# Kernel optimization log

Measured on AMD Instinct MI355X. Metric: run time of the kernel, lower is better.

The kernel has to match this reference:

```python
import jax, jax.numpy as jnp
import numpy as np

B = 32; N = 512; SEQ_LEN = 8
L = 0.05; T_REF = 5.0; V_TH = 20.0; V_RES = 0.0
SQL = float(np.sqrt(L))
BN_EPS = 1e-5

# ---- Dawson-style lookup tables for the LIF moment activation (built once, float64) ----
_XG = np.linspace(-10.0, 4.0, 7001)
_DX = _XG[1] - _XG[0]

def _cumtrapz(y):
    return np.concatenate([[0.0], np.cumsum(0.5 * (y[1:] + y[:-1]) * _DX)])

_phi = np.exp(-_XG ** 2)
_I = np.exp(-100.0) / 20.0 + _cumtrapz(_phi)          # int_{-inf}^x e^{-t^2} dt (asymptotic tail at -10)
_g = np.exp(_XG ** 2) * _I                             # 1st Dawson-like function g(x)
_G = _cumtrapz(_g)                                     # int g dx (rel. to -10)
_h = np.exp(_XG ** 2) * _cumtrapz(_phi * _g ** 2)      # 2nd Dawson-like function h(x)
_H = _cumtrapz(_h)                                     # int h dx

XG = jnp.asarray(_XG, jnp.float32)
GT = jnp.asarray(_g, jnp.float32)
GI = jnp.asarray(_G, jnp.float32)
HI = jnp.asarray(_H, jnp.float32)

def _interp(x, tab):
    return jnp.interp(x, XG, tab)

def moment_activate(u, s, rho):
    # Mnn_Activate_Mean / Std / Corr: LIF moment activation
    s = jnp.maximum(s, 1e-6)
    ub = jnp.clip((V_TH * L - u) / (s * SQL), -10.0, 4.0)
    lb = jnp.clip((V_RES * L - u) / (s * SQL), -10.0, 4.0)
    dG = _interp(ub, GI) - _interp(lb, GI)
    ua = 1.0 / (T_REF + (2.0 / L) * dG)                               # mean firing rate
    dH = jnp.maximum(_interp(ub, HI) - _interp(lb, HI), 0.0)
    sa = jnp.sqrt((8.0 / L ** 2) * dH * ua ** 3)                      # firing std
    dg = _interp(ub, GT) - _interp(lb, GT)
    chi = ua ** 2 * (2.0 / L) * dg / (SQL * jnp.maximum(sa, 1e-9))    # linear response coeff
    eye = jnp.eye(rho.shape[-1], dtype=rho.dtype)
    rho_out = chi[:, :, None] * chi[:, None, :] * rho                 # [B,N,N]
    rho_out = rho_out * (1.0 - eye) + eye                             # unit diagonal
    return ua, sa, rho_out

def linear_corr(W, b, u, s, rho):
    # Mnn_Linear_Corr: mean via affine map, covariance via W C W^T
    u_out = u @ W.T + b
    Cin = rho * s[:, :, None] * s[:, None, :]                         # [B,N,N] covariance
    C = jnp.einsum('bik,lk->bil', jnp.einsum('ij,bjk->bik', W, Cin), W)
    var = jnp.clip(jnp.diagonal(C, axis1=1, axis2=2), 0.0, None)
    s_out = jnp.sqrt(var)
    denom = s_out[:, :, None] * s_out[:, None, :]
    rho_out = jnp.where(denom > 1e-12, C / jnp.maximum(denom, 1e-12), 0.0)
    return u_out, s_out, rho_out

def mexi_hat(n, k=0.3):
    dx = 2.0 * np.pi / n
    x = np.arange(0.0, 2.0 * np.pi, dx)[:n]
    y = np.exp(2.0 * (np.cos(x) - 1.0)) * np.cos(2.0 * x)
    j = np.arange(n)
    idx = (j[None, :] - j[:, None]) % n                               # w[i,:] = y.roll(i)
    return y[idx].astype(np.float32)

def setup_inputs() -> dict:
    ks = jax.random.split(jax.random.key(0), 10)
    u = jax.random.normal(ks[0], (B, N), jnp.float32)
    s = jax.random.uniform(ks[1], (B, N), jnp.float32, 0.1, 1.0)
    A = jax.random.normal(ks[2], (B, N, N), jnp.float32) / np.sqrt(N)
    sym = 0.5 * (A + jnp.swapaxes(A, 1, 2))
    eye = jnp.eye(N, dtype=jnp.float32)
    rho = jnp.clip(sym, -0.5, 0.5) * (1.0 - eye) + eye                # valid-ish corr matrix
    u_ext = jax.random.normal(ks[3], (B, N), jnp.float32)
    s_ext = jax.random.uniform(ks[4], (B, N), jnp.float32, 0.1, 1.0)
    W = 0.02 * jax.random.normal(ks[5], (N, N), jnp.float32) + 0.1 * jnp.asarray(mexi_hat(N))
    b = 0.02 * jax.random.normal(ks[6], (N,), jnp.float32)
    W_ext = 0.02 * jax.random.normal(ks[7], (N, N), jnp.float32)
    b_ext = 0.02 * jax.random.normal(ks[8], (N,), jnp.float32)
    w_mean = 2.5 * jnp.ones((N,), jnp.float32)
    b_mean = 2.5 * jnp.ones((N,), jnp.float32)
    w_mean_ext = 2.5 * jnp.ones((N,), jnp.float32)
    b_mean_ext = 2.5 * jnp.ones((N,), jnp.float32)
    return {'u': u, 's': s, 'rho': rho, 'u_ext': u_ext, 's_ext': s_ext,
            'W': W, 'b': b, 'W_ext': W_ext, 'b_ext': b_ext,
            'w_mean': w_mean, 'b_mean': b_mean,
            'w_mean_ext': w_mean_ext, 'b_mean_ext': b_mean_ext,
            'seq_len': SEQ_LEN}

def reference(u, s, rho, u_ext, s_ext, W, b, W_ext, b_ext,
              w_mean, b_mean, w_mean_ext, b_mean_ext, seq_len):
    # external pathway (Mnn_Linear_without_Corr + BN), computed once
    u_e = u_ext @ W_ext.T + b_ext
    s_e = jnp.sqrt((s_ext ** 2) @ (W_ext ** 2).T)
    mean_e = jnp.mean(u_e, axis=0); var_e = jnp.var(u_e, axis=0)
    f_e = w_mean_ext / jnp.sqrt(var_e + BN_EPS)
    s_e = s_e * jnp.abs(f_e)                                          # Mnn_Std_Bn1d (uses pre-BN stats)
    u_e = (u_e - mean_e) * f_e + b_mean_ext

    def step(carry, _):
        u, s, rho = carry
        u, s, rho = linear_corr(W, b, u, s, rho)
        mean = jnp.mean(u, axis=0); var = jnp.var(u, axis=0)
        f = w_mean / jnp.sqrt(var + BN_EPS)
        s = s * jnp.abs(f)
        u = (u - mean) * f + b_mean
        u = u + u_e
        s = jnp.sqrt(s * s + s_e * s_e)
        return moment_activate(u, s, rho), None

    (u, s, rho), _ = jax.lax.scan(step, (u, s, rho), None, length=seq_len)
    return u, s, rho
```

## Files before the change

kernel.cpp:

```cpp
#include <hip/hip_runtime.h>
#include <math.h>


#define BB 32
#define NN 512
#define SEQ 8
#define TG 7001

typedef float f32x4 __attribute__((ext_vector_type(4)));
typedef short s16x8 __attribute__((ext_vector_type(8)));

__device__ __forceinline__ unsigned short bf16_rne(float v) {
    unsigned u = __float_as_uint(v);
    u += 0x7FFFu + ((u >> 16) & 1u);
    return (unsigned short)(u >> 16);
}
__device__ __forceinline__ float bf16_f(unsigned short h) {
    return __uint_as_float(((unsigned)h) << 16);
}
__device__ __forceinline__ void split2(float v, unsigned short& h, unsigned short& l) {
    unsigned short hh = bf16_rne(v);
    h = hh;
    l = bf16_rne(v - bf16_f(hh));
}

__device__ __forceinline__ size_t ts_idx(int r, int k) {
    return (size_t)(((r >> 4) * 16 + (k >> 5)) * 512 + ((k >> 3) & 3) * 128 + (r & 15) * 8 + (k & 7));
}

__device__ __forceinline__ float interp_tab(const float* __restrict__ tab, float x) {
    float t = (x + 10.0f) * 500.0f;
    t = fminf(fmaxf(t, 0.0f), 7000.0f);
    int i0 = (int)t;
    if (i0 > 6999) i0 = 6999;
    float fr = t - (float)i0;
    float a = tab[i0];
    float b = tab[i0 + 1];
    return a + fr * (b - a);
}

__global__ void k_exp(double* __restrict__ expP, double* __restrict__ expM) {
    int k = blockIdx.x * 256 + threadIdx.x;
    if (k >= TG) return;
    double x = -10.0 + (14.0 / 7000.0) * k;
    expP[k] = exp(x * x);
    expM[k] = exp(-x * x);
}

__device__ double blk_exscan(double part, double* wsum) {
    int t = threadIdx.x, lane = t & 63, wid = t >> 6;
    double run = part;
    #pragma unroll
    for (int off = 1; off < 64; off <<= 1) {
        double nv = __shfl_up(run, off);
        if (lane >= off) run += nv;
    }
    if (lane == 63) wsum[wid] = run;
    __syncthreads();
    if (t < 16) {
        double v = wsum[t];
        #pragma unroll
        for (int off = 1; off < 16; off <<= 1) {
            double nv = __shfl_up(v, off);
            if (lane >= off) v += nv;
        }
        wsum[t] = v;
    }
    __syncthreads();
    double base = (wid > 0) ? wsum[wid - 1] : 0.0;
    double ex = base + run - part;
    __syncthreads();
    return ex;
}

__global__ __launch_bounds__(1024)
void k_scan(const double* __restrict__ expP, const double* __restrict__ expM,
            float* __restrict__ GT, float* __restrict__ GI, float* __restrict__ HI) {
    __shared__ double ys[7008];
    __shared__ double wsum[16];
    const int t = threadIdx.x;
    const double dx = 14.0 / 7000.0;
    int k0 = t * 7, k1 = k0 + 7;
    if (k1 > TG) k1 = TG;
    if (k0 > TG) k0 = TG;
    int kls = (k0 < 1) ? 1 : k0;

    for (int k = k0; k < k1; ++k) ys[k] = expM[k];
    __syncthreads();

    double tmp[7];
    {
        double part = 0.0;
        for (int k = kls; k < k1; ++k) part += 0.5 * (ys[k - 1] + ys[k]) * dx;
        double run = blk_exscan(part, wsum) + exp(-100.0) / 20.0;
        int c = 0;
        for (int k = k0; k < k1; ++k) {
            if (k >= 1) run += 0.5 * (ys[k - 1] + ys[k]) * dx;
            tmp[c] = expP[k] * run;
            GT[k] = (float)tmp[c];
            ++c;
        }
        __syncthreads();
        c = 0;
        for (int k = k0; k < k1; ++k) ys[k] = tmp[c++];
        __syncthreads();
    }
    {
        double part = 0.0;
        for (int k = kls; k < k1; ++k) part += 0.5 * (ys[k - 1] + ys[k]) * dx;
        double run = blk_exscan(part, wsum);
        for (int k = k0; k < k1; ++k) {
            if (k >= 1) run += 0.5 * (ys[k - 1] + ys[k]) * dx;
            GI[k] = (float)run;
        }
        __syncthreads();
    }
    {
        double part = 0.0;
        for (int k = kls; k < k1; ++k) {
            double ya = expM[k - 1] * ys[k - 1] * ys[k - 1];
            double yb = expM[k] * ys[k] * ys[k];
            part += 0.5 * (ya + yb) * dx;
        }
        double run = blk_exscan(part, wsum);
        int c = 0;
        for (int k = k0; k < k1; ++k) {
            if (k >= 1) {
                double ya = expM[k - 1] * ys[k - 1] * ys[k - 1];
                double yb = expM[k] * ys[k] * ys[k];
                run += 0.5 * (ya + yb) * dx;
            }
            tmp[c++] = run;
        }
        __syncthreads();
        c = 0;
        for (int k = k0; k < k1; ++k) ys[k] = tmp[c++];
        __syncthreads();
    }
    {
        double part = 0.0;
        for (int k = kls; k < k1; ++k)
            part += 0.5 * (expP[k - 1] * ys[k - 1] + expP[k] * ys[k]) * dx;
        double run = blk_exscan(part, wsum);
        for (int k = k0; k < k1; ++k) {
            if (k >= 1) run += 0.5 * (expP[k - 1] * ys[k - 1] + expP[k] * ys[k]) * dx;
            HI[k] = (float)run;
        }
    }
}

__global__ void k_splitW(const float* __restrict__ W,
                         unsigned short* __restrict__ Wh, unsigned short* __restrict__ Wl) {
    int t = blockIdx.x * 256 + threadIdx.x;
    int r = t >> 6, c8 = t & 63;
    int k = c8 * 8;
    const float* src = W + (size_t)r * NN + k;
    s16x8 hv, lv;
    #pragma unroll
    for (int q = 0; q < 8; ++q) {
        unsigned short h, l;
        split2(src[q], h, l);
        hv[q] = (short)h; lv[q] = (short)l;
    }
    size_t o = ts_idx(r, k);
    *reinterpret_cast<s16x8*>(Wh + o) = hv;
    *reinterpret_cast<s16x8*>(Wl + o) = lv;
}

__global__ void k_splitQ(const float* __restrict__ rho, const float* __restrict__ s,
                         unsigned short* __restrict__ Qh, unsigned short* __restrict__ Ql) {
    int t = blockIdx.x * 256 + threadIdx.x;
    int b = t >> 15;
    int rem = t & 32767;
    int r = rem >> 6, c8 = rem & 63;
    int k = c8 * 8;
    const float* src = rho + ((size_t)b * NN + r) * NN + k;
    const float* sb = s + b * NN;
    float si = sb[r];
    s16x8 hv, lv;
    #pragma unroll
    for (int q = 0; q < 8; ++q) {
        float v = src[q] * si * sb[k + q];
        unsigned short h, l;
        split2(v, h, l);
        hv[q] = (short)h; lv[q] = (short)l;
    }
    size_t o = (size_t)b * NN * NN + ts_idx(r, k);
    *reinterpret_cast<s16x8*>(Qh + o) = hv;
    *reinterpret_cast<s16x8*>(Ql + o) = lv;
}

template <int PHASE>
__global__ __launch_bounds__(256, 2)
void gemm_ts(const unsigned short* __restrict__ Ah, const unsigned short* __restrict__ Al,
             long aStride,
             const unsigned short* __restrict__ Bh, const unsigned short* __restrict__ Bl,
             long bStride,
             unsigned short* __restrict__ Oh, unsigned short* __restrict__ Ol,
             float* __restrict__ Of,
             const float* __restrict__ Wf, float* __restrict__ sv_a, float* __restrict__ sv_b,
             const float* __restrict__ u_prev, const float* __restrict__ bvec,
             float* __restrict__ u_linT,
             const float* __restrict__ bn_w, const float* __restrict__ bmv,
             const float* __restrict__ u_e, const float* __restrict__ s_e2,
             const float* __restrict__ GT, const float* __restrict__ GI,
             const float* __restrict__ HI,
             float* __restrict__ u_next, float* __restrict__ s_next) {
    __shared__ __align__(16) unsigned short stg[4 * 8192];
    __shared__ float slS[256], chS[256], snS[256];

    const int id = blockIdx.x;
    const int member = (id >> 3) & 3;
    const int g = (id & 7) | ((id >> 5) << 3);
    const int p = g & 3;
    const int b = g >> 2;
    const int xt = (PHASE == 0) ? p : member;
    const int yt = (PHASE == 0) ? member : p;
    const int i0 = yt * 128, j0 = xt * 128;
    const int tid = threadIdx.x;
    const int w = tid >> 6, lane = tid & 63;
    const int wqm = w >> 1, wqn = w & 1;

    if (PHASE == 0) {
        const int tile16 = yt * 4 + xt;
        const int row = tile16 * 32 + (tid >> 3);
        const int seg = tid & 7;
        const float4* wr = (const float4*)(Wf + (size_t)row * NN + seg * 64);
        const float4* ur = (const float4*)(u_prev + b * NN + seg * 64);
        float a0 = 0.f, a1 = 0.f, a2 = 0.f, a3 = 0.f;
        #pragma unroll
        for (int kk = 0; kk < 16; ++kk) {
            float4 wv = wr[kk], uv = ur[kk];
            a0 = fmaf(wv.x, uv.x, a0);
            a1 = fmaf(wv.y, uv.y, a1);
            a2 = fmaf(wv.z, uv.z, a2);
            a3 = fmaf(wv.w, uv.w, a3);
        }
        float au = (a0 + a1) + (a2 + a3);
        au += __shfl_xor(au, 1);
        au += __shfl_xor(au, 2);
        au += __shfl_xor(au, 4);
        if (seg == 0) u_linT[row * BB + b] = au + bvec[row];
    } else {
        const int ii = (tid < 128) ? (i0 + tid) : (j0 + tid - 128);
        float vb[32];
        {
            const float4* ul = (const float4*)(u_linT + (size_t)ii * BB);
            #pragma unroll
            for (int q = 0; q < 8; ++q) {
                float4 t4 = ul[q];
                vb[q * 4 + 0] = t4.x; vb[q * 4 + 1] = t4.y;
                vb[q * 4 + 2] = t4.z; vb[q * 4 + 3] = t4.w;
            }
        }
        float m = 0.0f;
        #pragma unroll
        for (int bb = 0; bb < BB; ++bb) m += vb[bb];
        m *= (1.0f / BB);
        float v = 0.0f;
        #pragma unroll
        for (int bb = 0; bb < BB; ++bb) {
            float d = vb[bb] - m;
            v = fmaf(d, d, v);
        }
        v *= (1.0f / BB);
        float f = bn_w[ii] / sqrtf(v + 1e-5f);
        const int idx = b * NN + ii;
        float s_l = sqrtf(fmaxf(sv_a[idx], 0.0f));
        float un = (vb[b] - m) * f + bmv[ii] + u_e[idx];
        float sn = sqrtf(s_l * s_l * f * f + s_e2[idx]);
        const float SQL = 0.22360679774997896f;
        float ss = fmaxf(sn, 1e-6f);
        float inv = 1.0f / (ss * SQL);
        float ubx = fminf(fmaxf((1.0f - un) * inv, -10.0f), 4.0f);
        float lbx = fminf(fmaxf((0.0f - un) * inv, -10.0f), 4.0f);
        float dG = interp_tab(GI, ubx) - interp_tab(GI, lbx);
        float ua = 1.0f / (5.0f + 40.0f * dG);
        float dH = fmaxf(interp_tab(HI, ubx) - interp_tab(HI, lbx), 0.0f);
        float sa = sqrtf(3200.0f * dH * ua * ua * ua);
        float dg2 = interp_tab(GT, ubx) - interp_tab(GT, lbx);
        float ch = ua * ua * 40.0f * dg2 / (SQL * fmaxf(sa, 1e-9f));
        slS[tid] = s_l;
        chS[tid] = ch;
        snS[tid] = sa;
        if (i0 == j0 && tid < 128) {
            u_next[idx] = ua;
            s_next[idx] = sa;
            sv_b[idx] = 0.0f;
        }
        __syncthreads();
    }

    const int laneo = lane * 8;
    const unsigned short* pAh = Ah + (size_t)b * aStride + (size_t)((i0 >> 4) + wqm * 4) * 8192 + laneo;
    const unsigned short* pAl = Al + (size_t)b * aStride + (size_t)((i0 >> 4) + wqm * 4) * 8192 + laneo;
    const unsigned short* pBh = Bh + (size_t)b * bStride + (size_t)((j0 >> 4) + wqn * 4) * 8192 + laneo;
    const unsigned short* pBl = Bl + (size_t)b * bStride + (size_t)((j0 >> 4) + wqn * 4) * 8192 + laneo;

    f32x4 acc[4][4];
    #pragma unroll
    for (int m2 = 0; m2 < 4; ++m2)
        #pragma unroll
        for (int n2 = 0; n2 < 4; ++n2) acc[m2][n2] = (f32x4){0.f, 0.f, 0.f, 0.f};

    #pragma unroll 2
    for (int kb = 0; kb < 16; ++kb) {
        const int off = kb * 512;
        s16x8 ahf[4], alf[4], bhf[4], blf[4];
        #pragma unroll
        for (int t = 0; t < 4; ++t) {
            ahf[t] = *reinterpret_cast<const s16x8*>(pAh + t * 8192 + off);
            alf[t] = *reinterpret_cast<const s16x8*>(pAl + t * 8192 + off);
            bhf[t] = *reinterpret_cast<const s16x8*>(pBh + t * 8192 + off);
            blf[t] = *reinterpret_cast<const s16x8*>(pBl + t * 8192 + off);
        }
        #pragma unroll
        for (int m2 = 0; m2 < 4; ++m2)
            #pragma unroll
            for (int n2 = 0; n2 < 4; ++n2) {
                acc[m2][n2] = __builtin_amdgcn_mfma_f32_16x16x32_bf16(ahf[m2], bhf[n2], acc[m2][n2], 0, 0, 0);
                acc[m2][n2] = __builtin_amdgcn_mfma_f32_16x16x32_bf16(ahf[m2], blf[n2], acc[m2][n2], 0, 0, 0);
                acc[m2][n2] = __builtin_amdgcn_mfma_f32_16x16x32_bf16(alf[m2], bhf[n2], acc[m2][n2], 0, 0, 0);
            }
    }

    const size_t bofs = (size_t)b * NN * NN;
    const int rb0 = i0 + wqm * 64 + (lane >> 4) * 4;
    const int cb0 = j0 + wqn * 64 + (lane & 15);

    if (PHASE == 0) {
        float dp[16];
        #pragma unroll
        for (int m2 = 0; m2 < 4; ++m2)
            #pragma unroll
            for (int r = 0; r < 4; ++r) {
                int row = rb0 + m2 * 16 + r;
                const float* wrow = Wf + ((size_t)row << 9) + cb0;
                float s = 0.0f;
                #pragma unroll
                for (int n2 = 0; n2 < 4; ++n2) s = fmaf(acc[m2][n2][r], wrow[n2 * 16], s);
                dp[m2 * 4 + r] = s;
            }
        #pragma unroll
        for (int k = 0; k < 16; ++k) {
            #pragma unroll
            for (int off = 1; off < 16; off <<= 1) dp[k] += __shfl_xor(dp[k], off);
        }
        if ((lane & 15) == 0) {
            #pragma unroll
            for (int k = 0; k < 16; ++k) {
                int row = rb0 + (k >> 2) * 16 + (k & 3);
                atomicAdd(&sv_a[b * NN + row], dp[k]);
            }
        }
    }

    if (PHASE == 2) {
        float* fS = (float*)stg + w * 4096;
        const int lcf = ((lane >> 4) << 8) + (lane & 15);
        #pragma unroll
        for (int m2 = 0; m2 < 4; ++m2)
            #pragma unroll
            for (int r = 0; r < 4; ++r) {
                const int lr = m2 * 16 + (lane >> 4) * 4 + r;
                const float si = slS[wqm * 64 + lr], ci = chS[wqm * 64 + lr];
                const int row = i0 + wqm * 64 + lr;
                #pragma unroll
                for (int n2 = 0; n2 < 4; ++n2) {
                    const int lc = wqn * 64 + n2 * 16 + (lane & 15);
                    const float sj = slS[128 + lc], cj = chS[128 + lc];
                    const int col = j0 + lc;
                    float denom = si * sj;
                    float rv = (denom > 1e-12f) ? (acc[m2][n2][r] / fmaxf(denom, 1e-12f)) : 0.0f;
                    rv *= ci * cj;
                    if (row == col) rv = 1.0f;
                    fS[lcf + m2 * 1024 + r * 64 + n2 * 16] = rv;
                }
            }
        #pragma unroll
        for (int inst = 0; inst < 16; ++inst) {
            const int row = i0 + wqm * 64 + inst * 4 + (lane >> 4);
            const int col = j0 + wqn * 64 + (lane & 15) * 4;
            *reinterpret_cast<f32x4*>(Of + bofs + ((size_t)row << 9) + col) =
                *reinterpret_cast<const f32x4*>(fS + inst * 256 + (lane >> 4) * 64 + (lane & 15) * 4);
        }
    } else {
        unsigned short* hiS = stg + w * 8192;
        unsigned short* loS = hiS + 4096;
        const int laneconst = (((lane & 15) >> 3) << 7) + ((lane >> 4) << 5) + (lane & 7);
        #pragma unroll
        for (int m2 = 0; m2 < 4; ++m2)
            #pragma unroll
            for (int n2 = 0; n2 < 4; ++n2) {
                const int base = laneconst + m2 * 1024 + (n2 >> 1) * 512 + (n2 & 1) * 256;
                #pragma unroll
                for (int r = 0; r < 4; ++r) {
                    float v;
                    if (PHASE == 0) {
                        v = acc[m2][n2][r];
                    } else {
                        const int lr = wqm * 64 + m2 * 16 + (lane >> 4) * 4 + r;
                        const int lc = wqn * 64 + n2 * 16 + (lane & 15);
                        const float si = slS[lr], ci = chS[lr], qi = snS[lr];
                        const float sj = slS[128 + lc], cj = chS[128 + lc], qj = snS[128 + lc];
                        float denom = si * sj;
                        float rv = (denom > 1e-12f) ? (acc[m2][n2][r] / fmaxf(denom, 1e-12f)) : 0.0f;
                        rv *= ci * cj;
                        if (i0 + lr == j0 + lc) rv = 1.0f;
                        v = rv * qi * qj;
                    }
                    unsigned short h, l;
                    split2(v, h, l);
                    hiS[base + r * 8] = h;
                    loS[base + r * 8] = l;
                }
            }
        #pragma unroll
        for (int lb = 0; lb < 8; ++lb) {
            const int gb = ((i0 >> 4) + wqm * 4 + (lb >> 1)) * 16 + (j0 >> 5) + wqn * 2 + (lb & 1);
            *reinterpret_cast<s16x8*>(Oh + bofs + (size_t)gb * 512 + laneo) =
                *reinterpret_cast<const s16x8*>(hiS + lb * 512 + laneo);
            *reinterpret_cast<s16x8*>(Ol + bofs + (size_t)gb * 512 + laneo) =
                *reinterpret_cast<const s16x8*>(loS + lb * 512 + laneo);
        }
    }
}

__global__ void k_ext_dots(const float* __restrict__ Wx, const float* __restrict__ bx,
                           const float* __restrict__ ux, const float* __restrict__ sx,
                           float* __restrict__ u_e, float* __restrict__ s_e2) {
    int gw = (blockIdx.x << 2) + (threadIdx.x >> 6);
    int lane = threadIdx.x & 63;
    int b = gw >> 9, i = gw & 511;
    const float* wr = Wx + (size_t)i * NN;
    const float* ub = ux + b * NN;
    const float* sb = sx + b * NN;
    float au = 0.0f, as2 = 0.0f;
    for (int j = lane; j < NN; j += 64) {
        float w = wr[j];
        float s = sb[j];
        au = fmaf(w, ub[j], au);
        as2 = fmaf(w * w, s * s, as2);
    }
    #pragma unroll
    for (int off = 32; off; off >>= 1) {
        au += __shfl_down(au, off);
        as2 += __shfl_down(as2, off);
    }
    if (lane == 0) {
        u_e[b * NN + i] = au + bx[i];
        s_e2[b * NN + i] = as2;
    }
}

__global__ void k_ext_stats(float* __restrict__ u_e, float* __restrict__ s_e2,
                            const float* __restrict__ wmx, const float* __restrict__ bmx) {
    int i = blockIdx.x * blockDim.x + threadIdx.x;
    if (i >= NN) return;
    float m = 0.0f;
    for (int b = 0; b < BB; ++b) m += u_e[b * NN + i];
    m *= (1.0f / BB);
    float v = 0.0f;
    for (int b = 0; b < BB; ++b) {
        float d = u_e[b * NN + i] - m;
        v = fmaf(d, d, v);
    }
    v *= (1.0f / BB);
    float f = wmx[i] / sqrtf(v + 1e-5f);
    float bm = bmx[i];
    for (int b = 0; b < BB; ++b) {
        u_e[b * NN + i] = (u_e[b * NN + i] - m) * f + bm;
        s_e2[b * NN + i] *= f * f;
    }
}

extern "C" void kernel_launch(void* const* d_in, const int* in_sizes, int n_in,
                              void* d_out, int out_size, void* d_ws, size_t ws_size,
                              hipStream_t stream) {
    (void)in_sizes; (void)n_in; (void)out_size; (void)ws_size;
    const float* u_in       = (const float*)d_in[0];
    const float* s_in       = (const float*)d_in[1];
    const float* rho_in     = (const float*)d_in[2];
    const float* u_ext      = (const float*)d_in[3];
    const float* s_ext      = (const float*)d_in[4];
    const float* W          = (const float*)d_in[5];
    const float* bvec       = (const float*)d_in[6];
    const float* W_ext      = (const float*)d_in[7];
    const float* b_ext      = (const float*)d_in[8];
    const float* w_mean     = (const float*)d_in[9];
    const float* b_mean     = (const float*)d_in[10];
    const float* w_mean_ext = (const float*)d_in[11];
    const float* b_mean_ext = (const float*)d_in[12];

    float* out_u   = (float*)d_out;
    float* out_s   = out_u + BB * NN;
    float* out_rho = out_s + BB * NN;
    unsigned short* Qh = (unsigned short*)out_rho;
    unsigned short* Ql = Qh + (size_t)BB * NN * NN;

    char* base = (char*)d_ws;
    size_t off = 0;
    auto alloc = [&](size_t bytes) -> char* {
        char* ptr = base + off;
        off += (bytes + 255) & ~(size_t)255;
        return ptr;
    };
    unsigned short* T1h = (unsigned short*)alloc((size_t)BB * NN * NN * 2);
    unsigned short* T1l = (unsigned short*)alloc((size_t)BB * NN * NN * 2);
    unsigned short* Wh  = (unsigned short*)alloc((size_t)NN * NN * 2);
    unsigned short* Wl  = (unsigned short*)alloc((size_t)NN * NN * 2);
    double* expP = (double*)alloc(TG * 8);
    double* expM = (double*)alloc(TG * 8);
    float* GTt   = (float*)alloc(TG * 4);
    float* GIt   = (float*)alloc(TG * 4);
    float* HIt   = (float*)alloc(TG * 4);
    float* u_e   = (float*)alloc(BB * NN * 4);
    float* s_e2  = (float*)alloc(BB * NN * 4);
    float* uA    = (float*)alloc(BB * NN * 4);
    float* uB2   = (float*)alloc(BB * NN * 4);
    float* sA    = (float*)alloc(BB * NN * 4);
    float* sB2   = (float*)alloc(BB * NN * 4);
    float* u_linT = (float*)alloc(BB * NN * 4);
    float* sv0   = (float*)alloc(BB * NN * 4);
    float* sv1   = (float*)alloc(BB * NN * 4);

    k_exp<<<28, 256, 0, stream>>>(expP, expM);
    k_scan<<<1, 1024, 0, stream>>>(expP, expM, GTt, GIt, HIt);
    k_splitW<<<128, 256, 0, stream>>>(W, Wh, Wl);
    k_splitQ<<<4096, 256, 0, stream>>>(rho_in, s_in, Qh, Ql);
    k_ext_dots<<<BB * NN / 4, 256, 0, stream>>>(W_ext, b_ext, u_ext, s_ext, u_e, s_e2);
    k_ext_stats<<<2, 256, 0, stream>>>(u_e, s_e2, w_mean_ext, b_mean_ext);
    (void)hipMemsetAsync(sv0, 0, BB * NN * 4, stream);

    const float* cu = u_in;

    for (int t = 0; t < SEQ; ++t) {
        float* sva = (t & 1) ? sv1 : sv0;
        float* svb = (t & 1) ? sv0 : sv1;
        gemm_ts<0><<<512, 256, 0, stream>>>(
            Wh, Wl, 0L, Qh, Ql, (long)NN * NN, T1h, T1l, nullptr,
            W, sva, nullptr, cu, bvec, u_linT,
            nullptr, nullptr, nullptr, nullptr, nullptr, nullptr, nullptr,
            nullptr, nullptr);
        float* nu = (t == SEQ - 1) ? out_u : ((t & 1) ? uA : uB2);
        float* ns = (t == SEQ - 1) ? out_s : ((t & 1) ? sA : sB2);
        if (t < SEQ - 1) {
            gemm_ts<1><<<512, 256, 0, stream>>>(
                T1h, T1l, (long)NN * NN, Wh, Wl, 0L, Qh, Ql, nullptr,
                nullptr, sva, svb, nullptr, nullptr, u_linT,
                w_mean, b_mean, u_e, s_e2, GTt, GIt, HIt, nu, ns);
        } else {
            gemm_ts<2><<<512, 256, 0, stream>>>(
                T1h, T1l, (long)NN * NN, Wh, Wl, 0L, nullptr, nullptr, out_rho,
                nullptr, sva, svb, nullptr, nullptr, u_linT,
                w_mean, b_mean, u_e, s_e2, GTt, GIt, HIt, nu, ns);
        }
        cu = nu;
    }
}
```

Measured before the change: 759.4 us.

## Use 512-thread blocks with 8 waves per 128x128 tile and swizzled LDS staging

Doubles the threads per GEMM block from 256 to 512, so each of 8 waves computes a 64x32 sub-tile instead of 4 waves doing 64x64. This halves per-wave accumulators and B fragments, lowering register pressure and raising launch bounds to allow more resident waves. The epilogue staging layout is reworked with an XOR swizzle to reduce LDS bank conflicts, and the PHASE 0 mean dot product is split over 16 lanes. In exchange, A fragments are now loaded redundantly by more waves, and half the threads sit idle during the activation prologue.

Measured after the change: 803.4 us. 1.06x slower.

```diff
diff --git a/kernel.cpp b/kernel.cpp
--- a/kernel.cpp
+++ b/kernel.cpp
@@ -191,7 +191,7 @@
 }
 
 template <int PHASE>
-__global__ __launch_bounds__(256, 2)
+__global__ __launch_bounds__(512, 4)
 void gemm_ts(const unsigned short* __restrict__ Ah, const unsigned short* __restrict__ Al,
              long aStride,
              const unsigned short* __restrict__ Bh, const unsigned short* __restrict__ Bl,
@@ -206,7 +206,7 @@
              const float* __restrict__ GT, const float* __restrict__ GI,
              const float* __restrict__ HI,
              float* __restrict__ u_next, float* __restrict__ s_next) {
-    __shared__ __align__(16) unsigned short stg[4 * 8192];
+    __shared__ __align__(16) unsigned short stg[8 * 4096];
     __shared__ float slS[256], chS[256], snS[256];
 
     const int id = blockIdx.x;
@@ -219,17 +219,17 @@
     const int i0 = yt * 128, j0 = xt * 128;
     const int tid = threadIdx.x;
     const int w = tid >> 6, lane = tid & 63;
-    const int wqm = w >> 1, wqn = w & 1;
+    const int wqm = w >> 2, wqn = w & 3;
 
     if (PHASE == 0) {
         const int tile16 = yt * 4 + xt;
-        const int row = tile16 * 32 + (tid >> 3);
-        const int seg = tid & 7;
-        const float4* wr = (const float4*)(Wf + (size_t)row * NN + seg * 64);
-        const float4* ur = (const float4*)(u_prev + b * NN + seg * 64);
+        const int row = tile16 * 32 + (tid >> 4);
+        const int seg = tid & 15;
+        const float4* wr = (const float4*)(Wf + (size_t)row * NN + seg * 32);
+        const float4* ur = (const float4*)(u_prev + b * NN + seg * 32);
         float a0 = 0.f, a1 = 0.f, a2 = 0.f, a3 = 0.f;
         #pragma unroll
-        for (int kk = 0; kk < 16; ++kk) {
+        for (int kk = 0; kk < 8; ++kk) {
             float4 wv = wr[kk], uv = ur[kk];
             a0 = fmaf(wv.x, uv.x, a0);
             a1 = fmaf(wv.y, uv.y, a1);
@@ -240,53 +240,56 @@
         au += __shfl_xor(au, 1);
         au += __shfl_xor(au, 2);
         au += __shfl_xor(au, 4);
+        au += __shfl_xor(au, 8);
         if (seg == 0) u_linT[row * BB + b] = au + bvec[row];
     } else {
-        const int ii = (tid < 128) ? (i0 + tid) : (j0 + tid - 128);
-        float vb[32];
-        {
-            const float4* ul = (const float4*)(u_linT + (size_t)ii * BB);
-            #pragma unroll
-            for (int q = 0; q < 8; ++q) {
-                float4 t4 = ul[q];
-                vb[q * 4 + 0] = t4.x; vb[q * 4 + 1] = t4.y;
-                vb[q * 4 + 2] = t4.z; vb[q * 4 + 3] = t4.w;
-            }
-        }
-        float m = 0.0f;
-        #pragma unroll
-        for (int bb = 0; bb < BB; ++bb) m += vb[bb];
-        m *= (1.0f / BB);
-        float v = 0.0f;
-        #pragma unroll
-        for (int bb = 0; bb < BB; ++bb) {
-            float d = vb[bb] - m;
-            v = fmaf(d, d, v);
-        }
-        v *= (1.0f / BB);
-        float f = bn_w[ii] / sqrtf(v + 1e-5f);
-        const int idx = b * NN + ii;
-        float s_l = sqrtf(fmaxf(sv_a[idx], 0.0f));
-        float un = (vb[b] - m) * f + bmv[ii] + u_e[idx];
-        float sn = sqrtf(s_l * s_l * f * f + s_e2[idx]);
-        const float SQL = 0.22360679774997896f;
-        float ss = fmaxf(sn, 1e-6f);
-        float inv = 1.0f / (ss * SQL);
-        float ubx = fminf(fmaxf((1.0f - un) * inv, -10.0f), 4.0f);
-        float lbx = fminf(fmaxf((0.0f - un) * inv, -10.0f), 4.0f);
-        float dG = interp_tab(GI, ubx) - interp_tab(GI, lbx);
-        float ua = 1.0f / (5.0f + 40.0f * dG);
-        float dH = fmaxf(interp_tab(HI, ubx) - interp_tab(HI, lbx), 0.0f);
-        float sa = sqrtf(3200.0f * dH * ua * ua * ua);
-        float dg2 = interp_tab(GT, ubx) - interp_tab(GT, lbx);
-        float ch = ua * ua * 40.0f * dg2 / (SQL * fmaxf(sa, 1e-9f));
-        slS[tid] = s_l;
-        chS[tid] = ch;
-        snS[tid] = sa;
-        if (i0 == j0 && tid < 128) {
-            u_next[idx] = ua;
-            s_next[idx] = sa;
-            sv_b[idx] = 0.0f;
+        if (tid < 256) {
+            const int ii = (tid < 128) ? (i0 + tid) : (j0 + tid - 128);
+            float vb[32];
+            {
+                const float4* ul = (const float4*)(u_linT + (size_t)ii * BB);
+                #pragma unroll
+                for (int q = 0; q < 8; ++q) {
+                    float4 t4 = ul[q];
+                    vb[q * 4 + 0] = t4.x; vb[q * 4 + 1] = t4.y;
+                    vb[q * 4 + 2] = t4.z; vb[q * 4 + 3] = t4.w;
+                }
+            }
+            float m = 0.0f;
+            #pragma unroll
+            for (int bb = 0; bb < BB; ++bb) m += vb[bb];
+            m *= (1.0f / BB);
+            float v = 0.0f;
+            #pragma unroll
+            for (int bb = 0; bb < BB; ++bb) {
+                float d = vb[bb] - m;
+                v = fmaf(d, d, v);
+            }
+            v *= (1.0f / BB);
+            float f = bn_w[ii] / sqrtf(v + 1e-5f);
+            const int idx = b * NN + ii;
+            float s_l = sqrtf(fmaxf(sv_a[idx], 0.0f));
+            float un = (vb[b] - m) * f + bmv[ii] + u_e[idx];
+            float sn = sqrtf(s_l * s_l * f * f + s_e2[idx]);
+            const float SQL = 0.22360679774997896f;
+            float ss = fmaxf(sn, 1e-6f);
+            float inv = 1.0f / (ss * SQL);
+            float ubx = fminf(fmaxf((1.0f - un) * inv, -10.0f), 4.0f);
+            float lbx = fminf(fmaxf((0.0f - un) * inv, -10.0f), 4.0f);
+            float dG = interp_tab(GI, ubx) - interp_tab(GI, lbx);
+            float ua = 1.0f / (5.0f + 40.0f * dG);
+            float dH = fmaxf(interp_tab(HI, ubx) - interp_tab(HI, lbx), 0.0f);
+            float sa = sqrtf(3200.0f * dH * ua * ua * ua);
+            float dg2 = interp_tab(GT, ubx) - interp_tab(GT, lbx);
+            float ch = ua * ua * 40.0f * dg2 / (SQL * fmaxf(sa, 1e-9f));
+            slS[tid] = s_l;
+            chS[tid] = ch;
+            snS[tid] = sa;
+            if (i0 == j0 && tid < 128) {
+                u_next[idx] = ua;
+                s_next[idx] = sa;
+                sv_b[idx] = 0.0f;
+            }
         }
         __syncthreads();
     }
@@ -294,30 +297,33 @@
     const int laneo = lane * 8;
     const unsigned short* pAh = Ah + (size_t)b * aStride + (size_t)((i0 >> 4) + wqm * 4) * 8192 + laneo;
     const unsigned short* pAl = Al + (size_t)b * aStride + (size_t)((i0 >> 4) + wqm * 4) * 8192 + laneo;
-    const unsigned short* pBh = Bh + (size_t)b * bStride + (size_t)((j0 >> 4) + wqn * 4) * 8192 + laneo;
-    const unsigned short* pBl = Bl + (size_t)b * bStride + (size_t)((j0 >> 4) + wqn * 4) * 8192 + laneo;
-
-    f32x4 acc[4][4];
+    const unsigned short* pBh = Bh + (size_t)b * bStride + (size_t)((j0 >> 4) + wqn * 2) * 8192 + laneo;
+    const unsigned short* pBl = Bl + (size_t)b * bStride + (size_t)((j0 >> 4) + wqn * 2) * 8192 + laneo;
+
+    f32x4 acc[4][2];
     #pragma unroll
     for (int m2 = 0; m2 < 4; ++m2)
         #pragma unroll
-        for (int n2 = 0; n2 < 4; ++n2) acc[m2][n2] = (f32x4){0.f, 0.f, 0.f, 0.f};
+        for (int n2 = 0; n2 < 2; ++n2) acc[m2][n2] = (f32x4){0.f, 0.f, 0.f, 0.f};
 
     #pragma unroll 2
     for (int kb = 0; kb < 16; ++kb) {
         const int off = kb * 512;
-        s16x8 ahf[4], alf[4], bhf[4], blf[4];
+        s16x8 ahf[4], alf[4], bhf[2], blf[2];
         #pragma unroll
         for (int t = 0; t < 4; ++t) {
             ahf[t] = *reinterpret_cast<const s16x8*>(pAh + t * 8192 + off);
             alf[t] = *reinterpret_cast<const s16x8*>(pAl + t * 8192 + off);
+        }
+        #pragma unroll
+        for (int t = 0; t < 2; ++t) {
             bhf[t] = *reinterpret_cast<const s16x8*>(pBh + t * 8192 + off);
             blf[t] = *reinterpret_cast<const s16x8*>(pBl + t * 8192 + off);
         }
         #pragma unroll
         for (int m2 = 0; m2 < 4; ++m2)
             #pragma unroll
-            for (int n2 = 0; n2 < 4; ++n2) {
+            for (int n2 = 0; n2 < 2; ++n2) {
                 acc[m2][n2] = __builtin_amdgcn_mfma_f32_16x16x32_bf16(ahf[m2], bhf[n2], acc[m2][n2], 0, 0, 0);
                 acc[m2][n2] = __builtin_amdgcn_mfma_f32_16x16x32_bf16(ahf[m2], blf[n2], acc[m2][n2], 0, 0, 0);
                 acc[m2][n2] = __builtin_amdgcn_mfma_f32_16x16x32_bf16(alf[m2], bhf[n2], acc[m2][n2], 0, 0, 0);
@@ -325,10 +331,11 @@
     }
 
     const size_t bofs = (size_t)b * NN * NN;
-    const int rb0 = i0 + wqm * 64 + (lane >> 4) * 4;
-    const int cb0 = j0 + wqn * 64 + (lane & 15);
+    const int wq = lane >> 4;
 
     if (PHASE == 0) {
+        const int rb0 = i0 + wqm * 64 + wq * 4;
+        const int cb0 = j0 + wqn * 32 + (lane & 15);
         float dp[16];
         #pragma unroll
         for (int m2 = 0; m2 < 4; ++m2)
@@ -338,7 +345,7 @@
                 const float* wrow = Wf + ((size_t)row << 9) + cb0;
                 float s = 0.0f;
                 #pragma unroll
-                for (int n2 = 0; n2 < 4; ++n2) s = fmaf(acc[m2][n2][r], wrow[n2 * 16], s);
+                for (int n2 = 0; n2 < 2; ++n2) s = fmaf(acc[m2][n2][r], wrow[n2 * 16], s);
                 dp[m2 * 4 + r] = s;
             }
         #pragma unroll
@@ -356,51 +363,53 @@
     }
 
     if (PHASE == 2) {
-        float* fS = (float*)stg + w * 4096;
-        const int lcf = ((lane >> 4) << 8) + (lane & 15);
+        float* fS = (float*)stg + w * 2048;
         #pragma unroll
         for (int m2 = 0; m2 < 4; ++m2)
             #pragma unroll
             for (int r = 0; r < 4; ++r) {
-                const int lr = m2 * 16 + (lane >> 4) * 4 + r;
-                const float si = slS[wqm * 64 + lr], ci = chS[wqm * 64 + lr];
-                const int row = i0 + wqm * 64 + lr;
+                const int lr = wqm * 64 + m2 * 16 + wq * 4 + r;
+                const float si = slS[lr], ci = chS[lr];
+                const int row = i0 + lr;
                 #pragma unroll
-                for (int n2 = 0; n2 < 4; ++n2) {
-                    const int lc = wqn * 64 + n2 * 16 + (lane & 15);
+                for (int n2 = 0; n2 < 2; ++n2) {
+                    const int lc = wqn * 32 + n2 * 16 + (lane & 15);
                     const float sj = slS[128 + lc], cj = chS[128 + lc];
                     const int col = j0 + lc;
                     float denom = si * sj;
                     float rv = (denom > 1e-12f) ? (acc[m2][n2][r] / fmaxf(denom, 1e-12f)) : 0.0f;
                     rv *= ci * cj;
                     if (row == col) rv = 1.0f;
-                    fS[lcf + m2 * 1024 + r * 64 + n2 * 16] = rv;
+                    fS[(m2 * 16 + wq * 4 + r) * 32 + n2 * 16 + (lane & 15)] = rv;
                 }
             }
         #pragma unroll
-        for (int inst = 0; inst < 16; ++inst) {
-            const int row = i0 + wqm * 64 + inst * 4 + (lane >> 4);
-            const int col = j0 + wqn * 64 + (lane & 15) * 4;
+        for (int inst = 0; inst < 8; ++inst) {
+            const int lrow = inst * 8 + (lane >> 3);
+            const int lcol = (lane & 7) * 4;
+            const int row = i0 + wqm * 64 + lrow;
+            const int col = j0 + wqn * 32 + lcol;
             *reinterpret_cast<f32x4*>(Of + bofs + ((size_t)row << 9) + col) =
-                *reinterpret_cast<const f32x4*>(fS + inst * 256 + (lane >> 4) * 64 + (lane & 15) * 4);
+                *reinterpret_cast<const f32x4*>(fS + lrow * 32 + lcol);
         }
     } else {
-        unsigned short* hiS = stg + w * 8192;
-        unsigned short* loS = hiS + 4096;
-        const int laneconst = (((lane & 15) >> 3) << 7) + ((lane >> 4) << 5) + (lane & 7);
+        unsigned short* hiS = stg + w * 4096;
+        unsigned short* loS = hiS + 2048;
         #pragma unroll
         for (int m2 = 0; m2 < 4; ++m2)
             #pragma unroll
-            for (int n2 = 0; n2 < 4; ++n2) {
-                const int base = laneconst + m2 * 1024 + (n2 >> 1) * 512 + (n2 & 1) * 256;
+            for (int n2 = 0; n2 < 2; ++n2) {
+                const int cg = n2 * 2 + ((lane & 15) >> 3);
                 #pragma unroll
                 for (int r = 0; r < 4; ++r) {
+                    const int ribp = (wq << 2) | ((r ^ wq) & 3);
+                    const int base = m2 * 512 + cg * 128 + ribp * 8 + (lane & 7);
                     float v;
                     if (PHASE == 0) {
                         v = acc[m2][n2][r];
                     } else {
-                        const int lr = wqm * 64 + m2 * 16 + (lane >> 4) * 4 + r;
-                        const int lc = wqn * 64 + n2 * 16 + (lane & 15);
+                        const int lr = wqm * 64 + m2 * 16 + wq * 4 + r;
+                        const int lc = wqn * 32 + n2 * 16 + (lane & 15);
                         const float si = slS[lr], ci = chS[lr], qi = snS[lr];
                         const float sj = slS[128 + lc], cj = chS[128 + lc], qj = snS[128 + lc];
                         float denom = si * sj;
@@ -411,17 +420,18 @@
                     }
                     unsigned short h, l;
                     split2(v, h, l);
-                    hiS[base + r * 8] = h;
-                    loS[base + r * 8] = l;
+                    hiS[base] = h;
+                    loS[base] = l;
                 }
             }
-        #pragma unroll
-        for (int lb = 0; lb < 8; ++lb) {
-            const int gb = ((i0 >> 4) + wqm * 4 + (lb >> 1)) * 16 + (j0 >> 5) + wqn * 2 + (lb & 1);
+        const int cprm = (lane & 0x3C) | ((lane ^ (lane >> 2)) & 3);
+        #pragma unroll
+        for (int lb = 0; lb < 4; ++lb) {
+            const int gb = ((i0 >> 4) + wqm * 4 + lb) * 16 + (j0 >> 5) + wqn;
             *reinterpret_cast<s16x8*>(Oh + bofs + (size_t)gb * 512 + laneo) =
-                *reinterpret_cast<const s16x8*>(hiS + lb * 512 + laneo);
+                *reinterpret_cast<const s16x8*>(hiS + lb * 512 + cprm * 8);
             *reinterpret_cast<s16x8*>(Ol + bofs + (size_t)gb * 512 + laneo) =
-                *reinterpret_cast<const s16x8*>(loS + lb * 512 + laneo);
+                *reinterpret_cast<const s16x8*>(loS + lb * 512 + cprm * 8);
         }
     }
 }
@@ -537,7 +547,7 @@
     for (int t = 0; t < SEQ; ++t) {
         float* sva = (t & 1) ? sv1 : sv0;
         float* svb = (t & 1) ? sv0 : sv1;
-        gemm_ts<0><<<512, 256, 0, stream>>>(
+        gemm_ts<0><<<512, 512, 0, stream>>>(
             Wh, Wl, 0L, Qh, Ql, (long)NN * NN, T1h, T1l, nullptr,
             W, sva, nullptr, cu, bvec, u_linT,
             nullptr, nullptr, nullptr, nullptr, nullptr, nullptr, nullptr,
@@ -545,12 +555,12 @@
         float* nu = (t == SEQ - 1) ? out_u : ((t & 1) ? uA : uB2);
         float* ns = (t == SEQ - 1) ? out_s : ((t & 1) ? sA : sB2);
         if (t < SEQ - 1) {
-            gemm_ts<1><<<512, 256, 0, stream>>>(
+            gemm_ts<1><<<512, 512, 0, stream>>>(
                 T1h, T1l, (long)NN * NN, Wh, Wl, 0L, Qh, Ql, nullptr,
                 nullptr, sva, svb, nullptr, nullptr, u_linT,
                 w_mean, b_mean, u_e, s_e2, GTt, GIt, HIt, nu, ns);
         } else {
-            gemm_ts<2><<<512, 256, 0, stream>>>(
+            gemm_ts<2><<<512, 512, 0, stream>>>(
                 T1h, T1l, (long)NN * NN, Wh, Wl, 0L, nullptr, nullptr, out_rho,
                 nullptr, sva, svb, nullptr, nullptr, u_linT,
                 w_mean, b_mean, u_e, s_e2, GTt, GIt, HIt, nu, ns);
```
